# Optimization experiments

Measured on AMD Instinct MI355X. Metric: run time of the kernel, lower is better.

Reference implementation:

```python
import jax, jax.numpy as jnp
import numpy as np


def _leaky(x):
    return jnp.where(x >= 0, x, 0.01 * x)  # nn.LeakyReLU default slope


def _conv1x1(x, w):
    # x: [B, C, H, W], w: [O, C] (1x1 conv == per-pixel channel GEMM)
    return jnp.einsum('bchw,oc->bohw', x, w)


def setup_inputs() -> dict:
    key = jax.random.key(0)
    ks = jax.random.split(key, 12)

    def kaiming(k, o, c):  # kaiming_normal_ fan_out, relu gain, 1x1 kernel
        return jax.random.normal(k, (o, c), jnp.float32) * np.float32(np.sqrt(2.0 / o))

    lr_feature = jax.random.normal(ks[0], (1, 32, 256, 512), jnp.float32)
    hr_feature = jax.random.normal(ks[1], (1, 32, 512, 1024), jnp.float32)
    return {
        'lr_feature': lr_feature,
        'hr_feature': hr_feature,
        's1_w0': kaiming(ks[2], 128, 128),
        's1_w1': kaiming(ks[3], 64, 128),
        's1_w2': kaiming(ks[4], 32, 64),
        's1_w3': kaiming(ks[5], 16, 32),
        's1_w4': kaiming(ks[6], 8, 16),
        's1_w5': kaiming(ks[7], 1, 8),
        's2_w0': kaiming(ks[8], 3, 3),
        's2_w1': kaiming(ks[9], 2, 3),
        's2_w2': kaiming(ks[10], 1, 2),
        'fuse_w': jnp.ones((1, 2), jnp.float32),  # fuse weight initialized to 1
    }


def reference(lr_feature, hr_feature, s1_w0, s1_w1, s1_w2, s1_w3, s1_w4, s1_w5,
              s2_w0, s2_w1, s2_w2, fuse_w):
    scale = hr_feature.shape[-1] // lr_feature.shape[-1]  # static python int (=2, even)
    Hh, Wh = hr_feature.shape[-2], hr_feature.shape[-1]

    # nearest-neighbor upsample of lr_feature by `scale` (expand/view trick in torch)
    lr_up = jnp.repeat(jnp.repeat(lr_feature, scale, axis=2), scale, axis=3)

    # representation: [B, 128, Hh, Wh]
    rep = jnp.concatenate(
        [lr_up, hr_feature, lr_up * hr_feature, (lr_up - hr_feature) ** 2], axis=1)

    # similarity_measure1: 1x1-conv MLP chain 128->128->64->32->16->8->1
    o = _leaky(_conv1x1(rep, s1_w0))
    o = _leaky(_conv1x1(o, s1_w1))
    o = _leaky(_conv1x1(o, s1_w2))
    o = _leaky(_conv1x1(o, s1_w3))
    o = _conv1x1(o, s1_w4)
    weights1 = _conv1x1(o, s1_w5)  # [B, 1, Hh, Wh]

    # distance matrix (even-scale branch): 3 channels [dx, dy, norm]
    v = jnp.arange(-(scale // 2), scale // 2 + 1, dtype=jnp.float32)
    m = v.shape[0] // 2
    v = jnp.concatenate([v[:m], v[m + 1:]])  # drop center -> length `scale`
    d0 = jnp.broadcast_to(v[None, :], (scale, scale))
    dm = jnp.stack([d0, d0.T, jnp.sqrt(d0 ** 2 + d0.T ** 2)], axis=0)  # [3,s,s]
    dm = jnp.tile(dm, (1, Hh // scale, Wh // scale))[None]  # [1, 3, Hh, Wh]

    # similarity_measure2: 3->3->2->1
    w2 = _leaky(_conv1x1(dm, s2_w0))
    w2 = _leaky(_conv1x1(w2, s2_w1))
    weights2 = _conv1x1(w2, s2_w2)  # [1, 1, Hh, Wh]

    # fuse (weight forced non-negative via abs, as in forward's .data mutation)
    mapping = _conv1x1(jnp.concatenate([weights1, weights2], axis=1), jnp.abs(fuse_w))
    return mapping
```

## Files before the change

kernel.cpp:

```cpp
#include <hip/hip_runtime.h>

typedef short v8s __attribute__((ext_vector_type(8)));
typedef float v4f __attribute__((ext_vector_type(4)));

#define Wh   1024
#define Hh   512
#define HWh  (Wh * Hh)
#define Wlr  512
#define HWlr (Wlr * 256)
#define PAD  136
#define ITERS 8
#define NBLK  256

#define WFRAG_SHORTS (53 * 512)
#define ACT_SHORTS   (16 * PAD)
#define LDS_BYTES    ((WFRAG_SHORTS + 16 * ACT_SHORTS) * 2)

__device__ __forceinline__ unsigned short f2bf(float f) {
    union { float f; unsigned u; } v; v.f = f;
    unsigned r = v.u + 0x7FFFu + ((v.u >> 16) & 1u);
    return (unsigned short)(r >> 16);
}
__device__ __forceinline__ unsigned pk2(float a, float b) {
    union { float f; unsigned u; } ua, ub;
    ua.f = a; ub.f = b;
    return __builtin_amdgcn_perm(ub.u + 0x8000u, ua.u + 0x8000u, 0x07060302u);
}
__device__ __forceinline__ float leaky(float x) { return fmaxf(x, 0.01f * x); }

__global__ __launch_bounds__(1024, 4)
void cmfsm_kernel(const float* __restrict__ lr, const float* __restrict__ hr,
                  const float* __restrict__ w0g, const float* __restrict__ w1g,
                  const float* __restrict__ w2g, const float* __restrict__ w3g,
                  const float* __restrict__ w4g, const float* __restrict__ w5g,
                  const float* __restrict__ t0g, const float* __restrict__ t1g,
                  const float* __restrict__ t2g, const float* __restrict__ fwg,
                  float* __restrict__ out)
{
    extern __shared__ unsigned short smem[];
    unsigned short* wfrag = smem;
    unsigned short* actS  = smem + WFRAG_SHORTS;

    const int tid  = threadIdx.x;
    const int lane = tid & 63;
    const int wv   = tid >> 6;
    const int p    = lane & 15;
    const int q    = lane >> 4;

    for (int e = tid; e < 32 * 64; e += 1024) {
        int f = e >> 6, l = e & 63;
        int mt = f >> 2, ks = f & 3, pp = l & 15, qq = l >> 4;
        const float* src = w0g + (mt * 16 + pp) * 128 + ks * 32 + qq * 8;
        unsigned short* dst = wfrag + f * 512 + l * 8;
#pragma unroll
        for (int j = 0; j < 8; ++j) dst[j] = f2bf(src[j]);
    }
    if (tid < 16 * 64) {
        int f = tid >> 6, l = tid & 63;
        int mt = f >> 2, ks = f & 3, pp = l & 15, qq = l >> 4;
        const float* src = w1g + (mt * 16 + pp) * 128 + ks * 32 + qq * 8;
        unsigned short* dst = wfrag + (32 + f) * 512 + l * 8;
#pragma unroll
        for (int j = 0; j < 8; ++j) dst[j] = f2bf(src[j]);
    }
    if (tid < 4 * 64) {
        int f = tid >> 6, l = tid & 63;
        int mt = f >> 1, ks = f & 1, pp = l & 15, qq = l >> 4;
        const float* src = w2g + (mt * 16 + pp) * 64 + ks * 32 + qq * 8;
        unsigned short* dst = wfrag + (48 + f) * 512 + l * 8;
#pragma unroll
        for (int j = 0; j < 8; ++j) dst[j] = f2bf(src[j]);
    }
    if (tid < 64) {
        int l = tid;
        int pp = l & 15, qq = l >> 4;
        const float* src = w3g + pp * 32 + qq * 8;
        unsigned short* dst = wfrag + 52 * 512 + l * 8;
#pragma unroll
        for (int j = 0; j < 8; ++j) dst[j] = f2bf(src[j]);
    }

    float w45[4];
#pragma unroll
    for (int r = 0; r < 4; ++r) {
        float s = 0.f;
#pragma unroll
        for (int j = 0; j < 8; ++j) s += w5g[j] * w4g[j * 16 + q * 4 + r];
        w45[r] = s;
    }

    float w2tab[4];
#pragma unroll
    for (int yp = 0; yp < 2; ++yp)
#pragma unroll
        for (int xp = 0; xp < 2; ++xp) {
            float i0 = xp ? 1.f : -1.f;
            float i1 = yp ? 1.f : -1.f;
            float i2 = 1.41421356237309505f;
            float h0[3], h1[2];
            for (int o = 0; o < 3; ++o)
                h0[o] = leaky(t0g[o*3+0]*i0 + t0g[o*3+1]*i1 + t0g[o*3+2]*i2);
            for (int o = 0; o < 2; ++o)
                h1[o] = leaky(t1g[o*3+0]*h0[0] + t1g[o*3+1]*h0[1] + t1g[o*3+2]*h0[2]);
            w2tab[yp*2+xp] = t2g[0]*h1[0] + t2g[1]*h1[1];
        }
    const float fa = fabsf(fwg[0]);
    const float fb = fabsf(fwg[1]);

    __syncthreads();

    unsigned short* A = actS + wv * ACT_SHORTS;

    for (int it = 0; it < ITERS; ++it) {
        const int gbase = (blockIdx.x * ITERS + it) * 256 + wv * 16;
        const int y     = gbase >> 10;
        const int x0    = gbase & 1023;
        const int xg    = x0 + p;

#pragma unroll
        for (int pass = 0; pass < 4; ++pass) {
            int ch = pass * 8 + q * 2;
            const float* hp = hr + (size_t)ch * HWh + (size_t)y * Wh + xg;
            float h0 = hp[0];
            float h1 = hp[HWh];
            const float* lp = lr + (size_t)ch * HWlr + (size_t)(y >> 1) * Wlr + (xg >> 1);
            float l0 = lp[0];
            float l1 = lp[HWlr];
            unsigned* Ap = (unsigned*)(A + p * PAD);
            Ap[ch >> 1]        = pk2(l0, l1);
            Ap[(32 + ch) >> 1] = pk2(h0, h1);
            Ap[(64 + ch) >> 1] = pk2(l0 * h0, l1 * h1);
            float d0 = l0 - h0, d1 = l1 - h1;
            Ap[(96 + ch) >> 1] = pk2(d0 * d0, d1 * d1);
        }

        v4f acc0[8];
#pragma unroll
        for (int mt = 0; mt < 8; ++mt) acc0[mt] = (v4f){0.f, 0.f, 0.f, 0.f};
#pragma unroll
        for (int ks = 0; ks < 4; ++ks) {
            v8s b = *(const v8s*)(A + p * PAD + ks * 32 + q * 8);
#pragma unroll
            for (int mt = 0; mt < 8; ++mt) {
                v8s a = *(const v8s*)(wfrag + (mt * 4 + ks) * 512 + lane * 8);
                acc0[mt] = __builtin_amdgcn_mfma_f32_16x16x32_bf16(a, b, acc0[mt], 0, 0, 0);
            }
        }
#pragma unroll
        for (int mt = 0; mt < 8; ++mt) {
            uint2 v;
            v.x = pk2(leaky(acc0[mt][0]), leaky(acc0[mt][1]));
            v.y = pk2(leaky(acc0[mt][2]), leaky(acc0[mt][3]));
            *(uint2*)(A + p * PAD + mt * 16 + q * 4) = v;
        }

        v4f acc1[4];
#pragma unroll
        for (int mt = 0; mt < 4; ++mt) acc1[mt] = (v4f){0.f, 0.f, 0.f, 0.f};
#pragma unroll
        for (int ks = 0; ks < 4; ++ks) {
            v8s b = *(const v8s*)(A + p * PAD + ks * 32 + q * 8);
#pragma unroll
            for (int mt = 0; mt < 4; ++mt) {
                v8s a = *(const v8s*)(wfrag + (32 + mt * 4 + ks) * 512 + lane * 8);
                acc1[mt] = __builtin_amdgcn_mfma_f32_16x16x32_bf16(a, b, acc1[mt], 0, 0, 0);
            }
        }
#pragma unroll
        for (int mt = 0; mt < 4; ++mt) {
            uint2 v;
            v.x = pk2(leaky(acc1[mt][0]), leaky(acc1[mt][1]));
            v.y = pk2(leaky(acc1[mt][2]), leaky(acc1[mt][3]));
            *(uint2*)(A + p * PAD + mt * 16 + q * 4) = v;
        }

        v4f acc2[2];
#pragma unroll
        for (int mt = 0; mt < 2; ++mt) acc2[mt] = (v4f){0.f, 0.f, 0.f, 0.f};
#pragma unroll
        for (int ks = 0; ks < 2; ++ks) {
            v8s b = *(const v8s*)(A + p * PAD + ks * 32 + q * 8);
#pragma unroll
            for (int mt = 0; mt < 2; ++mt) {
                v8s a = *(const v8s*)(wfrag + (48 + mt * 2 + ks) * 512 + lane * 8);
                acc2[mt] = __builtin_amdgcn_mfma_f32_16x16x32_bf16(a, b, acc2[mt], 0, 0, 0);
            }
        }
#pragma unroll
        for (int mt = 0; mt < 2; ++mt) {
            uint2 v;
            v.x = pk2(leaky(acc2[mt][0]), leaky(acc2[mt][1]));
            v.y = pk2(leaky(acc2[mt][2]), leaky(acc2[mt][3]));
            *(uint2*)(A + p * PAD + mt * 16 + q * 4) = v;
        }

        {
            v8s b = *(const v8s*)(A + p * PAD + q * 8);
            v8s a = *(const v8s*)(wfrag + 52 * 512 + lane * 8);
            v4f acc3 = __builtin_amdgcn_mfma_f32_16x16x32_bf16(a, b, (v4f){0.f, 0.f, 0.f, 0.f}, 0, 0, 0);

            float part = 0.f;
#pragma unroll
            for (int r = 0; r < 4; ++r) part += w45[r] * leaky(acc3[r]);
            part += __shfl_xor(part, 16, 64);
            part += __shfl_xor(part, 32, 64);

            if (q == 0) {
                float res = fa * part + fb * w2tab[(y & 1) * 2 + (xg & 1)];
                out[y * Wh + xg] = res;
            }
        }
    }
}

extern "C" void kernel_launch(void* const* d_in, const int* in_sizes, int n_in,
                              void* d_out, int out_size, void* d_ws, size_t ws_size,
                              hipStream_t stream) {
    const float* lr  = (const float*)d_in[0];
    const float* hr  = (const float*)d_in[1];
    const float* w0g = (const float*)d_in[2];
    const float* w1g = (const float*)d_in[3];
    const float* w2g = (const float*)d_in[4];
    const float* w3g = (const float*)d_in[5];
    const float* w4g = (const float*)d_in[6];
    const float* w5g = (const float*)d_in[7];
    const float* t0g = (const float*)d_in[8];
    const float* t1g = (const float*)d_in[9];
    const float* t2g = (const float*)d_in[10];
    const float* fwg = (const float*)d_in[11];
    float* out = (float*)d_out;

    hipLaunchKernelGGL(cmfsm_kernel, dim3(NBLK), dim3(1024), LDS_BYTES, stream,
                       lr, hr, w0g, w1g, w2g, w3g, w4g, w5g, t0g, t1g, t2g, fwg, out);
}
```

Before: 149.5 us.

## Hold layer-0 weights in registers and process 32 pixels per wave

The first 128x128 layer's bf16 weight fragments now stay in VGPRs (32 v8s per lane) instead of being read from LDS for every MFMA. Each wave handles 32 pixels as two 16-pixel halves, so every weight fragment is reused across two MFMAs. Activations move to a fragment-native LDS layout with ping-pong buffers, so B operands load as contiguous per-lane vectors. Blocks drop to 512 threads, and the heavy register use (128 VGPRs for weights alone) risks lower occupancy.

Measured after the change: 233.4 us. +56.1%, slower.

```diff
diff --git a/kernel.cpp b/kernel.cpp
--- a/kernel.cpp
+++ b/kernel.cpp
@@ -8,13 +8,19 @@
 #define HWh  (Wh * Hh)
 #define Wlr  512
 #define HWlr (Wlr * 256)
-#define PAD  136
-#define ITERS 8
-#define NBLK  256
-
-#define WFRAG_SHORTS (53 * 512)
-#define ACT_SHORTS   (16 * PAD)
-#define LDS_BYTES    ((WFRAG_SHORTS + 16 * ACT_SHORTS) * 2)
+
+#define THREADS 512
+#define WAVES   8
+#define PXW     32
+#define NBLK    256
+#define ITERS   8
+
+#define HALF_STRIDE 2052
+#define BUF_STRIDE  (2 * HALF_STRIDE)
+#define ACT_SHORTS  (2 * BUF_STRIDE)
+#define WF_N        21
+#define WFRAG_SHORTS (WF_N * 512)
+#define LDS_BYTES   ((WFRAG_SHORTS + WAVES * ACT_SHORTS) * 2)
 
 __device__ __forceinline__ unsigned short f2bf(float f) {
     union { float f; unsigned u; } v; v.f = f;
@@ -28,7 +34,15 @@
 }
 __device__ __forceinline__ float leaky(float x) { return fmaxf(x, 0.01f * x); }
 
-__global__ __launch_bounds__(1024, 4)
+__device__ __forceinline__ void ep_write(unsigned short* buf, int h, int c0, int p, uint2 v) {
+    *(uint2*)(buf + h * HALF_STRIDE + (c0 >> 5) * 512 + (((c0 >> 3) & 3) * 16 + p) * 8 + (c0 & 7)) = v;
+}
+__device__ __forceinline__ void stage_pair(unsigned short* buf, int px, int rc, unsigned v) {
+    *(unsigned*)(buf + (px >> 4) * HALF_STRIDE + (rc >> 5) * 512 +
+                 (((rc >> 3) & 3) * 16 + (px & 15)) * 8 + (rc & 7)) = v;
+}
+
+__global__ __launch_bounds__(THREADS, 2)
 void cmfsm_kernel(const float* __restrict__ lr, const float* __restrict__ hr,
                   const float* __restrict__ w0g, const float* __restrict__ w1g,
                   const float* __restrict__ w2g, const float* __restrict__ w3g,
@@ -46,20 +60,14 @@
     const int wv   = tid >> 6;
     const int p    = lane & 15;
     const int q    = lane >> 4;
-
-    for (int e = tid; e < 32 * 64; e += 1024) {
+    const int px   = lane & 31;
+    const int cp   = lane >> 5;
+
+    for (int e = tid; e < 16 * 64; e += THREADS) {
         int f = e >> 6, l = e & 63;
         int mt = f >> 2, ks = f & 3, pp = l & 15, qq = l >> 4;
-        const float* src = w0g + (mt * 16 + pp) * 128 + ks * 32 + qq * 8;
+        const float* src = w1g + (mt * 16 + pp) * 128 + ks * 32 + qq * 8;
         unsigned short* dst = wfrag + f * 512 + l * 8;
-#pragma unroll
-        for (int j = 0; j < 8; ++j) dst[j] = f2bf(src[j]);
-    }
-    if (tid < 16 * 64) {
-        int f = tid >> 6, l = tid & 63;
-        int mt = f >> 2, ks = f & 3, pp = l & 15, qq = l >> 4;
-        const float* src = w1g + (mt * 16 + pp) * 128 + ks * 32 + qq * 8;
-        unsigned short* dst = wfrag + (32 + f) * 512 + l * 8;
 #pragma unroll
         for (int j = 0; j < 8; ++j) dst[j] = f2bf(src[j]);
     }
@@ -67,17 +75,27 @@
         int f = tid >> 6, l = tid & 63;
         int mt = f >> 1, ks = f & 1, pp = l & 15, qq = l >> 4;
         const float* src = w2g + (mt * 16 + pp) * 64 + ks * 32 + qq * 8;
-        unsigned short* dst = wfrag + (48 + f) * 512 + l * 8;
+        unsigned short* dst = wfrag + (16 + f) * 512 + l * 8;
 #pragma unroll
         for (int j = 0; j < 8; ++j) dst[j] = f2bf(src[j]);
     }
     if (tid < 64) {
-        int l = tid;
-        int pp = l & 15, qq = l >> 4;
+        int l = tid, pp = l & 15, qq = l >> 4;
         const float* src = w3g + pp * 32 + qq * 8;
-        unsigned short* dst = wfrag + 52 * 512 + l * 8;
+        unsigned short* dst = wfrag + 20 * 512 + l * 8;
 #pragma unroll
         for (int j = 0; j < 8; ++j) dst[j] = f2bf(src[j]);
+    }
+
+    v8s w0f[32];
+#pragma unroll
+    for (int f = 0; f < 32; ++f) {
+        int mt = f >> 2, ks = f & 3;
+        const float* src = w0g + (mt * 16 + p) * 128 + ks * 32 + q * 8;
+        v8s t;
+#pragma unroll
+        for (int j = 0; j < 8; ++j) t[j] = (short)f2bf(src[j]);
+        w0f[f] = t;
     }
 
     float w45[4];
@@ -109,106 +127,134 @@
 
     __syncthreads();
 
-    unsigned short* A = actS + wv * ACT_SHORTS;
+    unsigned short* actW = actS + wv * ACT_SHORTS;
+    unsigned short* B0 = actW;
+    unsigned short* B1 = actW + BUF_STRIDE;
+    const v4f z4 = (v4f){0.f, 0.f, 0.f, 0.f};
 
     for (int it = 0; it < ITERS; ++it) {
-        const int gbase = (blockIdx.x * ITERS + it) * 256 + wv * 16;
+        const int gbase = ((blockIdx.x * ITERS + it) * WAVES + wv) * PXW;
         const int y     = gbase >> 10;
         const int x0    = gbase & 1023;
-        const int xg    = x0 + p;
-
-#pragma unroll
-        for (int pass = 0; pass < 4; ++pass) {
-            int ch = pass * 8 + q * 2;
-            const float* hp = hr + (size_t)ch * HWh + (size_t)y * Wh + xg;
-            float h0 = hp[0];
-            float h1 = hp[HWh];
-            const float* lp = lr + (size_t)ch * HWlr + (size_t)(y >> 1) * Wlr + (xg >> 1);
-            float l0 = lp[0];
-            float l1 = lp[HWlr];
-            unsigned* Ap = (unsigned*)(A + p * PAD);
-            Ap[ch >> 1]        = pk2(l0, l1);
-            Ap[(32 + ch) >> 1] = pk2(h0, h1);
-            Ap[(64 + ch) >> 1] = pk2(l0 * h0, l1 * h1);
+        const float* hr_it = hr + gbase;
+        const float* lr_it = lr + (y >> 1) * Wlr + (x0 >> 1);
+
+#pragma unroll
+        for (int pass = 0; pass < 8; ++pass) {
+            const int ch = pass * 4 + cp * 2;
+            float h0 = hr_it[(size_t)ch * HWh + px];
+            float h1 = hr_it[(size_t)(ch + 1) * HWh + px];
+            float l0 = lr_it[(size_t)ch * HWlr + (px >> 1)];
+            float l1 = lr_it[(size_t)(ch + 1) * HWlr + (px >> 1)];
+            stage_pair(B0, px, ch,      pk2(l0, l1));
+            stage_pair(B0, px, 32 + ch, pk2(h0, h1));
+            stage_pair(B0, px, 64 + ch, pk2(l0 * h0, l1 * h1));
             float d0 = l0 - h0, d1 = l1 - h1;
-            Ap[(96 + ch) >> 1] = pk2(d0 * d0, d1 * d1);
-        }
-
-        v4f acc0[8];
-#pragma unroll
-        for (int mt = 0; mt < 8; ++mt) acc0[mt] = (v4f){0.f, 0.f, 0.f, 0.f};
-#pragma unroll
-        for (int ks = 0; ks < 4; ++ks) {
-            v8s b = *(const v8s*)(A + p * PAD + ks * 32 + q * 8);
-#pragma unroll
-            for (int mt = 0; mt < 8; ++mt) {
-                v8s a = *(const v8s*)(wfrag + (mt * 4 + ks) * 512 + lane * 8);
-                acc0[mt] = __builtin_amdgcn_mfma_f32_16x16x32_bf16(a, b, acc0[mt], 0, 0, 0);
-            }
-        }
-#pragma unroll
-        for (int mt = 0; mt < 8; ++mt) {
-            uint2 v;
-            v.x = pk2(leaky(acc0[mt][0]), leaky(acc0[mt][1]));
-            v.y = pk2(leaky(acc0[mt][2]), leaky(acc0[mt][3]));
-            *(uint2*)(A + p * PAD + mt * 16 + q * 4) = v;
-        }
-
-        v4f acc1[4];
-#pragma unroll
-        for (int mt = 0; mt < 4; ++mt) acc1[mt] = (v4f){0.f, 0.f, 0.f, 0.f};
-#pragma unroll
-        for (int ks = 0; ks < 4; ++ks) {
-            v8s b = *(const v8s*)(A + p * PAD + ks * 32 + q * 8);
+            stage_pair(B0, px, 96 + ch, pk2(d0 * d0, d1 * d1));
+        }
+
+#pragma unroll
+        for (int mh = 0; mh < 2; ++mh) {
+            v4f acc[4][2];
+#pragma unroll
+            for (int ks = 0; ks < 4; ++ks) {
+                v8s b0 = *(const v8s*)(B0 + ks * 512 + lane * 8);
+                v8s b1 = *(const v8s*)(B0 + HALF_STRIDE + ks * 512 + lane * 8);
+#pragma unroll
+                for (int mi = 0; mi < 4; ++mi) {
+                    const int f = (mh * 4 + mi) * 4 + ks;
+                    acc[mi][0] = __builtin_amdgcn_mfma_f32_16x16x32_bf16(
+                        w0f[f], b0, ks == 0 ? z4 : acc[mi][0], 0, 0, 0);
+                    acc[mi][1] = __builtin_amdgcn_mfma_f32_16x16x32_bf16(
+                        w0f[f], b1, ks == 0 ? z4 : acc[mi][1], 0, 0, 0);
+                }
+            }
+#pragma unroll
+            for (int mi = 0; mi < 4; ++mi) {
+                const int c0 = 16 * (mh * 4 + mi) + 4 * q;
+#pragma unroll
+                for (int h = 0; h < 2; ++h) {
+                    uint2 v;
+                    v.x = pk2(leaky(acc[mi][h][0]), leaky(acc[mi][h][1]));
+                    v.y = pk2(leaky(acc[mi][h][2]), leaky(acc[mi][h][3]));
+                    ep_write(B1, h, c0, p, v);
+                }
+            }
+        }
+
+        {
+            v4f acc[4][2];
+#pragma unroll
+            for (int ks = 0; ks < 4; ++ks) {
+                v8s b0 = *(const v8s*)(B1 + ks * 512 + lane * 8);
+                v8s b1 = *(const v8s*)(B1 + HALF_STRIDE + ks * 512 + lane * 8);
+#pragma unroll
+                for (int mt = 0; mt < 4; ++mt) {
+                    v8s a = *(const v8s*)(wfrag + (mt * 4 + ks) * 512 + lane * 8);
+                    acc[mt][0] = __builtin_amdgcn_mfma_f32_16x16x32_bf16(
+                        a, b0, ks == 0 ? z4 : acc[mt][0], 0, 0, 0);
+                    acc[mt][1] = __builtin_amdgcn_mfma_f32_16x16x32_bf16(
+                        a, b1, ks == 0 ? z4 : acc[mt][1], 0, 0, 0);
+                }
+            }
 #pragma unroll
             for (int mt = 0; mt < 4; ++mt) {
-                v8s a = *(const v8s*)(wfrag + (32 + mt * 4 + ks) * 512 + lane * 8);
-                acc1[mt] = __builtin_amdgcn_mfma_f32_16x16x32_bf16(a, b, acc1[mt], 0, 0, 0);
-            }
-        }
-#pragma unroll
-        for (int mt = 0; mt < 4; ++mt) {
-            uint2 v;
-            v.x = pk2(leaky(acc1[mt][0]), leaky(acc1[mt][1]));
-            v.y = pk2(leaky(acc1[mt][2]), leaky(acc1[mt][3]));
-            *(uint2*)(A + p * PAD + mt * 16 + q * 4) = v;
-        }
-
-        v4f acc2[2];
-#pragma unroll
-        for (int mt = 0; mt < 2; ++mt) acc2[mt] = (v4f){0.f, 0.f, 0.f, 0.f};
-#pragma unroll
-        for (int ks = 0; ks < 2; ++ks) {
-            v8s b = *(const v8s*)(A + p * PAD + ks * 32 + q * 8);
+                const int c0 = 16 * mt + 4 * q;
+#pragma unroll
+                for (int h = 0; h < 2; ++h) {
+                    uint2 v;
+                    v.x = pk2(leaky(acc[mt][h][0]), leaky(acc[mt][h][1]));
+                    v.y = pk2(leaky(acc[mt][h][2]), leaky(acc[mt][h][3]));
+                    ep_write(B0, h, c0, p, v);
+                }
+            }
+        }
+
+        {
+            v4f acc[2][2];
+#pragma unroll
+            for (int ks = 0; ks < 2; ++ks) {
+                v8s b0 = *(const v8s*)(B0 + ks * 512 + lane * 8);
+                v8s b1 = *(const v8s*)(B0 + HALF_STRIDE + ks * 512 + lane * 8);
+#pragma unroll
+                for (int mt = 0; mt < 2; ++mt) {
+                    v8s a = *(const v8s*)(wfrag + (16 + mt * 2 + ks) * 512 + lane * 8);
+                    acc[mt][0] = __builtin_amdgcn_mfma_f32_16x16x32_bf16(
+                        a, b0, ks == 0 ? z4 : acc[mt][0], 0, 0, 0);
+                    acc[mt][1] = __builtin_amdgcn_mfma_f32_16x16x32_bf16(
+                        a, b1, ks == 0 ? z4 : acc[mt][1], 0, 0, 0);
+                }
+            }
 #pragma unroll
             for (int mt = 0; mt < 2; ++mt) {
-                v8s a = *(const v8s*)(wfrag + (48 + mt * 2 + ks) * 512 + lane * 8);
-                acc2[mt] = __builtin_amdgcn_mfma_f32_16x16x32_bf16(a, b, acc2[mt], 0, 0, 0);
-            }
-        }
-#pragma unroll
-        for (int mt = 0; mt < 2; ++mt) {
-            uint2 v;
-            v.x = pk2(leaky(acc2[mt][0]), leaky(acc2[mt][1]));
-            v.y = pk2(leaky(acc2[mt][2]), leaky(acc2[mt][3]));
-            *(uint2*)(A + p * PAD + mt * 16 + q * 4) = v;
+                const int c0 = 16 * mt + 4 * q;
+#pragma unroll
+                for (int h = 0; h < 2; ++h) {
+                    uint2 v;
+                    v.x = pk2(leaky(acc[mt][h][0]), leaky(acc[mt][h][1]));
+                    v.y = pk2(leaky(acc[mt][h][2]), leaky(acc[mt][h][3]));
+                    ep_write(B1, h, c0, p, v);
+                }
+            }
         }
 
         {
-            v8s b = *(const v8s*)(A + p * PAD + q * 8);
-            v8s a = *(const v8s*)(wfrag + 52 * 512 + lane * 8);
-            v4f acc3 = __builtin_amdgcn_mfma_f32_16x16x32_bf16(a, b, (v4f){0.f, 0.f, 0.f, 0.f}, 0, 0, 0);
-
-            float part = 0.f;
-#pragma unroll
-            for (int r = 0; r < 4; ++r) part += w45[r] * leaky(acc3[r]);
-            part += __shfl_xor(part, 16, 64);
-            part += __shfl_xor(part, 32, 64);
-
-            if (q == 0) {
-                float res = fa * part + fb * w2tab[(y & 1) * 2 + (xg & 1)];
-                out[y * Wh + xg] = res;
-            }
+            v8s a = *(const v8s*)(wfrag + 20 * 512 + lane * 8);
+            float res[2];
+#pragma unroll
+            for (int h = 0; h < 2; ++h) {
+                v8s b = *(const v8s*)(B1 + h * HALF_STRIDE + lane * 8);
+                v4f acc3 = __builtin_amdgcn_mfma_f32_16x16x32_bf16(a, b, z4, 0, 0, 0);
+                float part = 0.f;
+#pragma unroll
+                for (int r = 0; r < 4; ++r) part += w45[r] * leaky(acc3[r]);
+                part += __shfl_xor(part, 16, 64);
+                part += __shfl_xor(part, 32, 64);
+                res[h] = part;
+            }
+            const float wb = fb * w2tab[((y & 1) << 1) | (p & 1)];
+            if (q == 0)      out[gbase + p]      = fa * res[0] + wb;
+            else if (q == 1) out[gbase + 16 + p] = fa * res[1] + wb;
         }
     }
 }
@@ -230,6 +276,6 @@
     const float* fwg = (const float*)d_in[11];
     float* out = (float*)d_out;
 
-    hipLaunchKernelGGL(cmfsm_kernel, dim3(NBLK), dim3(1024), LDS_BYTES, stream,
+    hipLaunchKernelGGL(cmfsm_kernel, dim3(NBLK), dim3(THREADS), LDS_BYTES, stream,
                        lr, hr, w0g, w1g, w2g, w3g, w4g, w5g, t0g, t1g, t2g, fwg, out);
 }
```

## Keep MLP activations in registers via ds_bpermute transpose instead of LDS staging

Applied to the files above, without the earlier changes.

Each layer's MFMA output is now turned into the next layer's B-operand layout with ds_bpermute lane shuffles, so the per-wave LDS activation buffer and its store/load round trips go away. Input channels are loaded directly into B fragments, with each lane taking 8 consecutive channels. With LDS use reduced to just the weight fragments, the launch doubles the block count, halves iterations per block and raises the occupancy hint. The cost is more VGPR pressure and extra permute instructions, and the ds_bpermute mapping must match the MFMA layout exactly.

Result: slower. 584.8 us (+291.2%).

```diff
diff --git a/kernel.cpp b/kernel.cpp
--- a/kernel.cpp
+++ b/kernel.cpp
@@ -4,17 +4,15 @@
 typedef float v4f __attribute__((ext_vector_type(4)));
 
 #define Wh   1024
-#define Hh   512
-#define HWh  (Wh * Hh)
+#define HWh  (1024 * 512)
 #define Wlr  512
-#define HWlr (Wlr * 256)
-#define PAD  136
-#define ITERS 8
-#define NBLK  256
+#define HWlr (512 * 256)
+
+#define THREADS 1024
+#define NBLK    512
+#define ITERS   4
 
 #define WFRAG_SHORTS (53 * 512)
-#define ACT_SHORTS   (16 * PAD)
-#define LDS_BYTES    ((WFRAG_SHORTS + 16 * ACT_SHORTS) * 2)
 
 __device__ __forceinline__ unsigned short f2bf(float f) {
     union { float f; unsigned u; } v; v.f = f;
@@ -28,7 +26,25 @@
 }
 __device__ __forceinline__ float leaky(float x) { return fmaxf(x, 0.01f * x); }
 
-__global__ __launch_bounds__(1024, 4)
+__device__ __forceinline__ v8s xpose(unsigned a0, unsigned a1, unsigned b0, unsigned b1,
+                                     int adr0, int adr1, bool low) {
+    unsigned r0a = __builtin_amdgcn_ds_bpermute(adr0, a0);
+    unsigned r0b = __builtin_amdgcn_ds_bpermute(adr0, b0);
+    unsigned r1a = __builtin_amdgcn_ds_bpermute(adr0, a1);
+    unsigned r1b = __builtin_amdgcn_ds_bpermute(adr0, b1);
+    unsigned r2a = __builtin_amdgcn_ds_bpermute(adr1, a0);
+    unsigned r2b = __builtin_amdgcn_ds_bpermute(adr1, b0);
+    unsigned r3a = __builtin_amdgcn_ds_bpermute(adr1, a1);
+    unsigned r3b = __builtin_amdgcn_ds_bpermute(adr1, b1);
+    union { uint4 u; v8s s; } c;
+    c.u.x = low ? r0a : r0b;
+    c.u.y = low ? r1a : r1b;
+    c.u.z = low ? r2a : r2b;
+    c.u.w = low ? r3a : r3b;
+    return c.s;
+}
+
+__global__ __launch_bounds__(THREADS, 8)
 void cmfsm_kernel(const float* __restrict__ lr, const float* __restrict__ hr,
                   const float* __restrict__ w0g, const float* __restrict__ w1g,
                   const float* __restrict__ w2g, const float* __restrict__ w3g,
@@ -37,9 +53,7 @@
                   const float* __restrict__ t2g, const float* __restrict__ fwg,
                   float* __restrict__ out)
 {
-    extern __shared__ unsigned short smem[];
-    unsigned short* wfrag = smem;
-    unsigned short* actS  = smem + WFRAG_SHORTS;
+    __shared__ unsigned short wfrag[WFRAG_SHORTS];
 
     const int tid  = threadIdx.x;
     const int lane = tid & 63;
@@ -47,7 +61,7 @@
     const int p    = lane & 15;
     const int q    = lane >> 4;
 
-    for (int e = tid; e < 32 * 64; e += 1024) {
+    for (int e = tid; e < 32 * 64; e += THREADS) {
         int f = e >> 6, l = e & 63;
         int mt = f >> 2, ks = f & 3, pp = l & 15, qq = l >> 4;
         const float* src = w0g + (mt * 16 + pp) * 128 + ks * 32 + qq * 8;
@@ -55,7 +69,7 @@
 #pragma unroll
         for (int j = 0; j < 8; ++j) dst[j] = f2bf(src[j]);
     }
-    if (tid < 16 * 64) {
+    {
         int f = tid >> 6, l = tid & 63;
         int mt = f >> 2, ks = f & 3, pp = l & 15, qq = l >> 4;
         const float* src = w1g + (mt * 16 + pp) * 128 + ks * 32 + qq * 8;
@@ -72,8 +86,7 @@
         for (int j = 0; j < 8; ++j) dst[j] = f2bf(src[j]);
     }
     if (tid < 64) {
-        int l = tid;
-        int pp = l & 15, qq = l >> 4;
+        int l = tid, pp = l & 15, qq = l >> 4;
         const float* src = w3g + pp * 32 + qq * 8;
         unsigned short* dst = wfrag + 52 * 512 + l * 8;
 #pragma unroll
@@ -107,97 +120,113 @@
     const float fa = fabsf(fwg[0]);
     const float fb = fabsf(fwg[1]);
 
+    const int adr0 = ((((2 * q) + 0) & 3) * 16 + p) << 2;
+    const int adr1 = ((((2 * q) + 1) & 3) * 16 + p) << 2;
+    const bool low = (q < 2);
+
     __syncthreads();
-
-    unsigned short* A = actS + wv * ACT_SHORTS;
-
+    const v4f z4 = (v4f){0.f, 0.f, 0.f, 0.f};
+
+#pragma unroll 1
     for (int it = 0; it < ITERS; ++it) {
         const int gbase = (blockIdx.x * ITERS + it) * 256 + wv * 16;
         const int y     = gbase >> 10;
-        const int x0    = gbase & 1023;
-        const int xg    = x0 + p;
-
-#pragma unroll
-        for (int pass = 0; pass < 4; ++pass) {
-            int ch = pass * 8 + q * 2;
-            const float* hp = hr + (size_t)ch * HWh + (size_t)y * Wh + xg;
-            float h0 = hp[0];
-            float h1 = hp[HWh];
-            const float* lp = lr + (size_t)ch * HWlr + (size_t)(y >> 1) * Wlr + (xg >> 1);
-            float l0 = lp[0];
-            float l1 = lp[HWlr];
-            unsigned* Ap = (unsigned*)(A + p * PAD);
-            Ap[ch >> 1]        = pk2(l0, l1);
-            Ap[(32 + ch) >> 1] = pk2(h0, h1);
-            Ap[(64 + ch) >> 1] = pk2(l0 * h0, l1 * h1);
-            float d0 = l0 - h0, d1 = l1 - h1;
-            Ap[(96 + ch) >> 1] = pk2(d0 * d0, d1 * d1);
-        }
-
-        v4f acc0[8];
-#pragma unroll
-        for (int mt = 0; mt < 8; ++mt) acc0[mt] = (v4f){0.f, 0.f, 0.f, 0.f};
-#pragma unroll
-        for (int ks = 0; ks < 4; ++ks) {
-            v8s b = *(const v8s*)(A + p * PAD + ks * 32 + q * 8);
-#pragma unroll
-            for (int mt = 0; mt < 8; ++mt) {
-                v8s a = *(const v8s*)(wfrag + (mt * 4 + ks) * 512 + lane * 8);
-                acc0[mt] = __builtin_amdgcn_mfma_f32_16x16x32_bf16(a, b, acc0[mt], 0, 0, 0);
-            }
-        }
-#pragma unroll
-        for (int mt = 0; mt < 8; ++mt) {
-            uint2 v;
-            v.x = pk2(leaky(acc0[mt][0]), leaky(acc0[mt][1]));
-            v.y = pk2(leaky(acc0[mt][2]), leaky(acc0[mt][3]));
-            *(uint2*)(A + p * PAD + mt * 16 + q * 4) = v;
-        }
-
-        v4f acc1[4];
-#pragma unroll
-        for (int mt = 0; mt < 4; ++mt) acc1[mt] = (v4f){0.f, 0.f, 0.f, 0.f};
-#pragma unroll
-        for (int ks = 0; ks < 4; ++ks) {
-            v8s b = *(const v8s*)(A + p * PAD + ks * 32 + q * 8);
+        const int xg    = (gbase & 1023) + p;
+
+        float h[8], l[8];
+        {
+            const float* hb = hr + (size_t)y * Wh + xg;
+            const float* lb = lr + (size_t)(y >> 1) * Wlr + (xg >> 1);
+#pragma unroll
+            for (int j = 0; j < 8; ++j) {
+                h[j] = hb[(size_t)(8 * q + j) * HWh];
+                l[j] = lb[(size_t)(8 * q + j) * HWlr];
+            }
+        }
+        v8s bfr[4];
+        {
+            unsigned* b0 = (unsigned*)&bfr[0];
+            unsigned* b1 = (unsigned*)&bfr[1];
+            unsigned* b2 = (unsigned*)&bfr[2];
+            unsigned* b3 = (unsigned*)&bfr[3];
+#pragma unroll
+            for (int jj = 0; jj < 4; ++jj) {
+                float l0 = l[2*jj], l1 = l[2*jj+1];
+                float h0 = h[2*jj], h1 = h[2*jj+1];
+                b0[jj] = pk2(l0, l1);
+                b1[jj] = pk2(h0, h1);
+                b2[jj] = pk2(l0 * h0, l1 * h1);
+                float d0 = l0 - h0, d1 = l1 - h1;
+                b3[jj] = pk2(d0 * d0, d1 * d1);
+            }
+        }
+
+        v8s nb[4];
+#pragma unroll
+        for (int mh = 0; mh < 2; ++mh) {
+            v4f acc[4];
+#pragma unroll
+            for (int ks = 0; ks < 4; ++ks)
+#pragma unroll
+                for (int mi = 0; mi < 4; ++mi) {
+                    v8s a = *(const v8s*)(wfrag + ((mh * 4 + mi) * 4 + ks) * 512 + lane * 8);
+                    acc[mi] = __builtin_amdgcn_mfma_f32_16x16x32_bf16(
+                        a, bfr[ks], ks == 0 ? z4 : acc[mi], 0, 0, 0);
+                }
+            unsigned pd[4][2];
+#pragma unroll
+            for (int mi = 0; mi < 4; ++mi) {
+                pd[mi][0] = pk2(leaky(acc[mi][0]), leaky(acc[mi][1]));
+                pd[mi][1] = pk2(leaky(acc[mi][2]), leaky(acc[mi][3]));
+            }
+            nb[2*mh + 0] = xpose(pd[0][0], pd[0][1], pd[1][0], pd[1][1], adr0, adr1, low);
+            nb[2*mh + 1] = xpose(pd[2][0], pd[2][1], pd[3][0], pd[3][1], adr0, adr1, low);
+        }
+
+        v8s b2f[2];
+        {
+            v4f acc[4];
+#pragma unroll
+            for (int ks = 0; ks < 4; ++ks)
+#pragma unroll
+                for (int mt = 0; mt < 4; ++mt) {
+                    v8s a = *(const v8s*)(wfrag + (32 + mt * 4 + ks) * 512 + lane * 8);
+                    acc[mt] = __builtin_amdgcn_mfma_f32_16x16x32_bf16(
+                        a, nb[ks], ks == 0 ? z4 : acc[mt], 0, 0, 0);
+                }
+            unsigned pd[4][2];
 #pragma unroll
             for (int mt = 0; mt < 4; ++mt) {
-                v8s a = *(const v8s*)(wfrag + (32 + mt * 4 + ks) * 512 + lane * 8);
-                acc1[mt] = __builtin_amdgcn_mfma_f32_16x16x32_bf16(a, b, acc1[mt], 0, 0, 0);
-            }
-        }
-#pragma unroll
-        for (int mt = 0; mt < 4; ++mt) {
-            uint2 v;
-            v.x = pk2(leaky(acc1[mt][0]), leaky(acc1[mt][1]));
-            v.y = pk2(leaky(acc1[mt][2]), leaky(acc1[mt][3]));
-            *(uint2*)(A + p * PAD + mt * 16 + q * 4) = v;
-        }
-
-        v4f acc2[2];
-#pragma unroll
-        for (int mt = 0; mt < 2; ++mt) acc2[mt] = (v4f){0.f, 0.f, 0.f, 0.f};
-#pragma unroll
-        for (int ks = 0; ks < 2; ++ks) {
-            v8s b = *(const v8s*)(A + p * PAD + ks * 32 + q * 8);
+                pd[mt][0] = pk2(leaky(acc[mt][0]), leaky(acc[mt][1]));
+                pd[mt][1] = pk2(leaky(acc[mt][2]), leaky(acc[mt][3]));
+            }
+            b2f[0] = xpose(pd[0][0], pd[0][1], pd[1][0], pd[1][1], adr0, adr1, low);
+            b2f[1] = xpose(pd[2][0], pd[2][1], pd[3][0], pd[3][1], adr0, adr1, low);
+        }
+
+        v8s b3f;
+        {
+            v4f acc[2];
+#pragma unroll
+            for (int ks = 0; ks < 2; ++ks)
+#pragma unroll
+                for (int mt = 0; mt < 2; ++mt) {
+                    v8s a = *(const v8s*)(wfrag + (48 + mt * 2 + ks) * 512 + lane * 8);
+                    acc[mt] = __builtin_amdgcn_mfma_f32_16x16x32_bf16(
+                        a, b2f[ks], ks == 0 ? z4 : acc[mt], 0, 0, 0);
+                }
+            unsigned pd[2][2];
 #pragma unroll
             for (int mt = 0; mt < 2; ++mt) {
-                v8s a = *(const v8s*)(wfrag + (48 + mt * 2 + ks) * 512 + lane * 8);
-                acc2[mt] = __builtin_amdgcn_mfma_f32_16x16x32_bf16(a, b, acc2[mt], 0, 0, 0);
-            }
-        }
-#pragma unroll
-        for (int mt = 0; mt < 2; ++mt) {
-            uint2 v;
-            v.x = pk2(leaky(acc2[mt][0]), leaky(acc2[mt][1]));
-            v.y = pk2(leaky(acc2[mt][2]), leaky(acc2[mt][3]));
-            *(uint2*)(A + p * PAD + mt * 16 + q * 4) = v;
-        }
-
-        {
-            v8s b = *(const v8s*)(A + p * PAD + q * 8);
+                pd[mt][0] = pk2(leaky(acc[mt][0]), leaky(acc[mt][1]));
+                pd[mt][1] = pk2(leaky(acc[mt][2]), leaky(acc[mt][3]));
+            }
+            b3f = xpose(pd[0][0], pd[0][1], pd[1][0], pd[1][1], adr0, adr1, low);
+        }
+
+        {
             v8s a = *(const v8s*)(wfrag + 52 * 512 + lane * 8);
-            v4f acc3 = __builtin_amdgcn_mfma_f32_16x16x32_bf16(a, b, (v4f){0.f, 0.f, 0.f, 0.f}, 0, 0, 0);
+            v4f acc3 = __builtin_amdgcn_mfma_f32_16x16x32_bf16(a, b3f, z4, 0, 0, 0);
 
             float part = 0.f;
 #pragma unroll
@@ -206,8 +235,7 @@
             part += __shfl_xor(part, 32, 64);
 
             if (q == 0) {
-                float res = fa * part + fb * w2tab[(y & 1) * 2 + (xg & 1)];
-                out[y * Wh + xg] = res;
+                out[y * Wh + xg] = fa * part + fb * w2tab[((y & 1) << 1) | (xg & 1)];
             }
         }
     }
@@ -230,6 +258,6 @@
     const float* fwg = (const float*)d_in[11];
     float* out = (float*)d_out;
 
-    hipLaunchKernelGGL(cmfsm_kernel, dim3(NBLK), dim3(1024), LDS_BYTES, stream,
+    hipLaunchKernelGGL(cmfsm_kernel, dim3(NBLK), dim3(THREADS), 0, stream,
                        lr, hr, w0g, w1g, w2g, w3g, w4g, w5g, t0g, t1g, t2g, fwg, out);
 }
```
